# Kernel tuning notes

Measured on AMD Instinct MI355X. Metric: run time of the kernel, lower is better.

Reference implementation:

```python
import jax, jax.numpy as jnp
import numpy as np
import math

B, N, C = 8, 2048, 512

def setup_inputs() -> dict:
    key = jax.random.key(0)
    ks = jax.random.split(key, 7)
    s = 1.0 / math.sqrt(C)
    return {
        "feature": jax.random.normal(ks[0], (B, N, C), dtype=jnp.float32),
        "wq": jax.random.uniform(ks[1], (C, C), jnp.float32, -s, s),
        "bq": jax.random.uniform(ks[2], (C,), jnp.float32, -s, s),
        "wk": jax.random.uniform(ks[3], (C, C), jnp.float32, -s, s),
        "bk": jax.random.uniform(ks[4], (C,), jnp.float32, -s, s),
        "wv": jax.random.uniform(ks[5], (C, C), jnp.float32, -s, s),
        "bv": jax.random.uniform(ks[6], (C,), jnp.float32, -s, s),
    }

def reference(feature, wq, bq, wk, bk, wv, bv):
    # torch nn.Linear: x @ W.T + b
    q = jnp.einsum('bnc,dc->bnd', feature, wq) + bq
    k = jnp.einsum('bnc,dc->bnd', feature, wk) + bk
    v = jnp.einsum('bnc,dc->bnd', feature, wv) + bv
    scores = jnp.einsum('bnd,bmd->bnm', q, k)          # [B, N, N]
    attn = jax.nn.softmax(scores, axis=2) / math.sqrt(C)  # post-softmax scale (as in source)
    v_star = jnp.einsum('bnm,bmd->bnd', attn, v)
    return feature + v_star
```

## Files before the change

kernel.cpp:

```cpp
#include <hip/hip_runtime.h>
#include <cstdint>
#include <cstddef>


typedef __bf16 bf16x8 __attribute__((ext_vector_type(8)));
typedef float f32x4 __attribute__((ext_vector_type(4)));
typedef short short4v __attribute__((ext_vector_type(4)));
typedef short short8v __attribute__((ext_vector_type(8)));

__device__ __forceinline__ float b2f(short s) {
  union { float f; unsigned u; } u; u.u = ((unsigned)(unsigned short)s) << 16; return u.f;
}
__device__ __forceinline__ short f2b(float f) {
  union { float f; unsigned u; } u; u.f = f;
  unsigned r = (u.u + 0x7fffu + ((u.u >> 16) & 1u)) >> 16;
  return (short)r;
}

#define GLDS(gptr, lptr) \
  __builtin_amdgcn_global_load_lds( \
      (const __attribute__((address_space(1))) unsigned int*)(const void*)(gptr), \
      (__attribute__((address_space(3))) unsigned int*)(void*)(lptr), 16, 0, 0)

__global__ __launch_bounds__(256) void cvt_f32_bf16(const float* __restrict__ src,
                                                    short* __restrict__ dst, int n4) {
  int i = blockIdx.x * 256 + threadIdx.x;
  if (i >= n4) return;
  float4 f = ((const float4*)src)[i];
  short4v o = { f2b(f.x), f2b(f.y), f2b(f.z), f2b(f.w) };
  *(short4v*)(dst + (size_t)i * 4) = o;
}

__global__ __launch_bounds__(256) void cvt_w3(const float* __restrict__ w0,
                                              const float* __restrict__ w1,
                                              const float* __restrict__ w2,
                                              short* __restrict__ dst) {
  int i = blockIdx.x * 256 + threadIdx.x;
  const float* src = (i < 65536) ? w0 : (i < 131072) ? w1 : w2;
  int loc = i & 65535;
  float4 f = ((const float4*)src)[loc];
  short4v o = { f2b(f.x), f2b(f.y), f2b(f.z), f2b(f.w) };
  *(short4v*)(dst + (size_t)i * 4) = o;
}

__global__ __launch_bounds__(256) void pack_bias(const float* __restrict__ b0,
                                                 const float* __restrict__ b1,
                                                 const float* __restrict__ b2,
                                                 float* __restrict__ dst) {
  int t = blockIdx.x * 256 + threadIdx.x;
  if (t >= 1536) return;
  const float* s = (t < 512) ? b0 : (t < 1024) ? b1 : b2;
  dst[t] = s[t & 511];
}

__global__ __launch_bounds__(256) void gemm_qkv(const short* __restrict__ A,
                                                const short* __restrict__ Wb,
                                                const float* __restrict__ biasP,
                                                short* __restrict__ Out) {
  __shared__ __align__(16) short As[128 * 32];
  __shared__ __align__(16) short Bs[128 * 32];
  const int z = blockIdx.z;
  const short* Bm = Wb + (size_t)z * 262144;
  const int m0 = blockIdx.y * 128, n0 = blockIdx.x * 128;
  const int t = threadIdx.x;
  const int lane = t & 63, w = t >> 6;
  const int wm = (w & 1) * 64, wn = (w >> 1) * 64;
  const int fr = lane & 15, fk = (lane >> 4) * 8;

  f32x4 acc[4][4] = {};
  const int c0 = t, c1 = t + 256;
  const int r0 = c0 >> 2, k80 = (c0 & 3) * 8;
  const int r1 = c1 >> 2, k81 = (c1 & 3) * 8;

  for (int k0 = 0; k0 < 512; k0 += 32) {
    __syncthreads();
    GLDS(A + (size_t)(m0 + r0) * 512 + k0 + k80, As + c0 * 8);
    GLDS(A + (size_t)(m0 + r1) * 512 + k0 + k81, As + c1 * 8);
    GLDS(Bm + (size_t)(n0 + r0) * 512 + k0 + k80, Bs + c0 * 8);
    GLDS(Bm + (size_t)(n0 + r1) * 512 + k0 + k81, Bs + c1 * 8);
    __syncthreads();
    bf16x8 a[4], b[4];
#pragma unroll
    for (int i = 0; i < 4; ++i) a[i] = *(const bf16x8*)(As + (wm + i * 16 + fr) * 32 + fk);
#pragma unroll
    for (int j = 0; j < 4; ++j) b[j] = *(const bf16x8*)(Bs + (wn + j * 16 + fr) * 32 + fk);
#pragma unroll
    for (int i = 0; i < 4; ++i)
#pragma unroll
      for (int j = 0; j < 4; ++j)
        acc[i][j] = __builtin_amdgcn_mfma_f32_16x16x32_bf16(a[i], b[j], acc[i][j], 0, 0, 0);
  }

  const int rq = (lane >> 4) * 4;
#pragma unroll
  for (int i = 0; i < 4; ++i)
#pragma unroll
    for (int j = 0; j < 4; ++j)
#pragma unroll
      for (int r = 0; r < 4; ++r) {
        int row = m0 + wm + i * 16 + rq + r;
        int col = n0 + wn + j * 16 + fr;
        Out[(size_t)z * 8388608 + (size_t)row * 512 + col] =
            f2b(acc[i][j][r] + biasP[z * 512 + col]);
      }
}

__global__ __launch_bounds__(256) void gemm_qk(const short* __restrict__ Q,
                                               const short* __restrict__ K,
                                               short* __restrict__ P,
                                               float* __restrict__ l) {
  __shared__ __align__(16) short As[128 * 32];
  __shared__ __align__(16) short Bs[128 * 32];
  const int z = blockIdx.z;
  const short* A = Q + (size_t)z * 2048 * 512;
  const short* Bm = K + (size_t)z * 2048 * 512;
  const int m0 = blockIdx.y * 128, n0 = blockIdx.x * 128;
  const int t = threadIdx.x;
  const int lane = t & 63, w = t >> 6;
  const int wm = (w & 1) * 64, wn = (w >> 1) * 64;
  const int fr = lane & 15, fk = (lane >> 4) * 8;

  f32x4 acc[4][4] = {};
  const int c0 = t, c1 = t + 256;
  const int r0 = c0 >> 2, k80 = (c0 & 3) * 8;
  const int r1 = c1 >> 2, k81 = (c1 & 3) * 8;

  for (int k0 = 0; k0 < 512; k0 += 32) {
    __syncthreads();
    GLDS(A + (size_t)(m0 + r0) * 512 + k0 + k80, As + c0 * 8);
    GLDS(A + (size_t)(m0 + r1) * 512 + k0 + k81, As + c1 * 8);
    GLDS(Bm + (size_t)(n0 + r0) * 512 + k0 + k80, Bs + c0 * 8);
    GLDS(Bm + (size_t)(n0 + r1) * 512 + k0 + k81, Bs + c1 * 8);
    __syncthreads();
    bf16x8 a[4], b[4];
#pragma unroll
    for (int i = 0; i < 4; ++i) a[i] = *(const bf16x8*)(As + (wm + i * 16 + fr) * 32 + fk);
#pragma unroll
    for (int j = 0; j < 4; ++j) b[j] = *(const bf16x8*)(Bs + (wn + j * 16 + fr) * 32 + fk);
#pragma unroll
    for (int i = 0; i < 4; ++i)
#pragma unroll
      for (int j = 0; j < 4; ++j)
        acc[i][j] = __builtin_amdgcn_mfma_f32_16x16x32_bf16(a[i], b[j], acc[i][j], 0, 0, 0);
  }

  const int rq = (lane >> 4) * 4;
  float rs[4][4];
#pragma unroll
  for (int i = 0; i < 4; ++i)
#pragma unroll
    for (int r = 0; r < 4; ++r) rs[i][r] = 0.f;

#pragma unroll
  for (int i = 0; i < 4; ++i)
#pragma unroll
    for (int j = 0; j < 4; ++j)
#pragma unroll
      for (int r = 0; r < 4; ++r) {
        int row = m0 + wm + i * 16 + rq + r;
        int col = n0 + wn + j * 16 + fr;
        float e = exp2f(acc[i][j][r] * 1.4426950408889634f);
        short eb = f2b(e);
        P[(size_t)z * 4194304 + (size_t)row * 2048 + col] = eb;
        rs[i][r] += b2f(eb);
      }
#pragma unroll
  for (int i = 0; i < 4; ++i)
#pragma unroll
    for (int r = 0; r < 4; ++r) {
#pragma unroll
      for (int m = 1; m < 16; m <<= 1) rs[i][r] += __shfl_xor(rs[i][r], m);
    }
  if (fr == 0) {
#pragma unroll
    for (int i = 0; i < 4; ++i)
#pragma unroll
      for (int r = 0; r < 4; ++r)
        atomicAdd(&l[z * 2048 + m0 + wm + i * 16 + rq + r], rs[i][r]);
  }
}

__global__ __launch_bounds__(256) void gemm_pv(const short* __restrict__ Pm,
                                               const short* __restrict__ Vt,
                                               const float* __restrict__ l,
                                               const float* __restrict__ resid,
                                               float* __restrict__ out, float scale) {
  __shared__ __align__(16) short As[64 * 32];
  __shared__ __align__(16) short Bs[128 * 32];
  const int z = blockIdx.z;
  const short* A = Pm + (size_t)z * 4194304;
  const short* Bm = Vt + (size_t)z * 1048576;
  const int m0 = blockIdx.y * 64, n0 = blockIdx.x * 128;
  const int t = threadIdx.x;
  const int lane = t & 63, w = t >> 6;
  const int wm = (w & 1) * 32, wn = (w >> 1) * 64;
  const int fr = lane & 15, fk = (lane >> 4) * 8;

  f32x4 acc[2][4] = {};
  const int ra = t >> 2, k8a = (t & 3) * 8;
  const int c0 = t, c1 = t + 256;
  const int r0 = c0 >> 2, k80 = (c0 & 3) * 8;
  const int r1 = c1 >> 2, k81 = (c1 & 3) * 8;

  for (int k0 = 0; k0 < 2048; k0 += 32) {
    __syncthreads();
    GLDS(A + (size_t)(m0 + ra) * 2048 + k0 + k8a, As + t * 8);
    GLDS(Bm + (size_t)(n0 + r0) * 2048 + k0 + k80, Bs + c0 * 8);
    GLDS(Bm + (size_t)(n0 + r1) * 2048 + k0 + k81, Bs + c1 * 8);
    __syncthreads();
    bf16x8 a[2], b[4];
#pragma unroll
    for (int i = 0; i < 2; ++i) a[i] = *(const bf16x8*)(As + (wm + i * 16 + fr) * 32 + fk);
#pragma unroll
    for (int j = 0; j < 4; ++j) b[j] = *(const bf16x8*)(Bs + (wn + j * 16 + fr) * 32 + fk);
#pragma unroll
    for (int i = 0; i < 2; ++i)
#pragma unroll
      for (int j = 0; j < 4; ++j)
        acc[i][j] = __builtin_amdgcn_mfma_f32_16x16x32_bf16(a[i], b[j], acc[i][j], 0, 0, 0);
  }

  const int rq = (lane >> 4) * 4;
#pragma unroll
  for (int i = 0; i < 2; ++i)
#pragma unroll
    for (int r = 0; r < 4; ++r) {
      int row = m0 + wm + i * 16 + rq + r;
      float linv = scale / l[z * 2048 + row];
#pragma unroll
      for (int j = 0; j < 4; ++j) {
        int col = n0 + wn + j * 16 + fr;
        size_t idx = (size_t)z * 1048576 + (size_t)row * 512 + col;
        out[idx] = resid[idx] + acc[i][j][r] * linv;
      }
    }
}

__global__ __launch_bounds__(256) void transpose64(const short* __restrict__ V,
                                                   short* __restrict__ Vt) {
  __shared__ short tile[64][72];
  const int b = blockIdx.z;
  const int d0 = blockIdx.x * 64, n0 = blockIdx.y * 64;
  const int t = threadIdx.x;
#pragma unroll
  for (int h = 0; h < 2; ++h) {
    int c = t + h * 256;
    int r = c >> 3, cj = (c & 7) * 8;
    short8v val = *(const short8v*)(V + ((size_t)(b * 2048 + n0 + r)) * 512 + d0 + cj);
#pragma unroll
    for (int j = 0; j < 8; ++j) tile[r][cj + j] = val[j];
  }
  __syncthreads();
#pragma unroll
  for (int h = 0; h < 2; ++h) {
    int c = t + h * 256;
    int dr = c >> 3, nj = (c & 7) * 8;
    short8v o;
#pragma unroll
    for (int j = 0; j < 8; ++j) o[j] = tile[nj + j][dr];
    *(short8v*)(Vt + ((size_t)b * 512 + d0 + dr) * 2048 + n0 + nj) = o;
  }
}

extern "C" void kernel_launch(void* const* d_in, const int* in_sizes, int n_in,
                              void* d_out, int out_size, void* d_ws, size_t ws_size,
                              hipStream_t stream) {
  const float* feature = (const float*)d_in[0];
  const float* wq = (const float*)d_in[1];
  const float* bq = (const float*)d_in[2];
  const float* wk = (const float*)d_in[3];
  const float* bk = (const float*)d_in[4];
  const float* wv = (const float*)d_in[5];
  const float* bv = (const float*)d_in[6];
  float* out = (float*)d_out;

  const size_t MN = (size_t)16384 * 512;
  short* Xb = (short*)d_ws;
  short* Wb = Xb + MN;
  short* Q = Wb + 786432;
  short* K = Q + MN;
  short* V = K + MN;
  short* Vt = V + MN;
  short* P = Vt + MN;
  float* biasP = (float*)(P + (size_t)8 * 2048 * 2048);
  float* l = biasP + 1536;

  cvt_f32_bf16<<<8192, 256, 0, stream>>>(feature, Xb, 2097152);
  cvt_w3<<<768, 256, 0, stream>>>(wq, wk, wv, Wb);
  pack_bias<<<6, 256, 0, stream>>>(bq, bk, bv, biasP);
  hipMemsetAsync(l, 0, 16384 * sizeof(float), stream);

  gemm_qkv<<<dim3(4, 128, 3), 256, 0, stream>>>(Xb, Wb, biasP, Q);
  transpose64<<<dim3(8, 32, 8), 256, 0, stream>>>(V, Vt);
  gemm_qk<<<dim3(16, 16, 8), 256, 0, stream>>>(Q, K, P, l);

  const float iscl = 0.044194173824159216f;
  gemm_pv<<<dim3(4, 32, 8), 256, 0, stream>>>(P, Vt, l, feature, out, iscl);
}
```

Before: 277.3 us.

## Swap MFMA operands for vectorized row-contiguous epilogue stores and fuse prep kernels

Merges the three conversion/bias kernels and the memset into one prep launch, removing several launches. In the three GEMMs it swaps the MFMA A/B operands so each lane's four accumulator values lie along contiguous output columns. This allows 8-byte bf16 and 16-byte float4 epilogue stores and loads instead of scalar strided ones. The row-sum reduction in gemm_qk now needs only two shuffles plus atomics from 16 lanes.

```diff
diff --git a/kernel.cpp b/kernel.cpp
--- a/kernel.cpp
+++ b/kernel.cpp
@@ -22,49 +22,52 @@
       (const __attribute__((address_space(1))) unsigned int*)(const void*)(gptr), \
       (__attribute__((address_space(3))) unsigned int*)(void*)(lptr), 16, 0, 0)
 
-__global__ __launch_bounds__(256) void cvt_f32_bf16(const float* __restrict__ src,
-                                                    short* __restrict__ dst, int n4) {
-  int i = blockIdx.x * 256 + threadIdx.x;
-  if (i >= n4) return;
-  float4 f = ((const float4*)src)[i];
-  short4v o = { f2b(f.x), f2b(f.y), f2b(f.z), f2b(f.w) };
-  *(short4v*)(dst + (size_t)i * 4) = o;
-}
-
-__global__ __launch_bounds__(256) void cvt_w3(const float* __restrict__ w0,
-                                              const float* __restrict__ w1,
-                                              const float* __restrict__ w2,
-                                              short* __restrict__ dst) {
-  int i = blockIdx.x * 256 + threadIdx.x;
-  const float* src = (i < 65536) ? w0 : (i < 131072) ? w1 : w2;
-  int loc = i & 65535;
-  float4 f = ((const float4*)src)[loc];
-  short4v o = { f2b(f.x), f2b(f.y), f2b(f.z), f2b(f.w) };
-  *(short4v*)(dst + (size_t)i * 4) = o;
-}
-
-__global__ __launch_bounds__(256) void pack_bias(const float* __restrict__ b0,
-                                                 const float* __restrict__ b1,
-                                                 const float* __restrict__ b2,
-                                                 float* __restrict__ dst) {
-  int t = blockIdx.x * 256 + threadIdx.x;
-  if (t >= 1536) return;
-  const float* s = (t < 512) ? b0 : (t < 1024) ? b1 : b2;
-  dst[t] = s[t & 511];
-}
-
-__global__ __launch_bounds__(256) void gemm_qkv(const short* __restrict__ A,
-                                                const short* __restrict__ Wb,
+__global__ __launch_bounds__(256) void prep(const float* __restrict__ f,
+                                            const float* __restrict__ w0,
+                                            const float* __restrict__ w1,
+                                            const float* __restrict__ w2,
+                                            const float* __restrict__ b0,
+                                            const float* __restrict__ b1,
+                                            const float* __restrict__ b2,
+                                            short* __restrict__ Xb, short* __restrict__ Wb,
+                                            float* __restrict__ biasP, float* __restrict__ l) {
+  const int bid = blockIdx.x;
+  const int t = threadIdx.x;
+  if (bid < 8192) {
+    int i = bid * 256 + t;
+    float4 v = ((const float4*)f)[i];
+    short4v o = { f2b(v.x), f2b(v.y), f2b(v.z), f2b(v.w) };
+    *(short4v*)(Xb + (size_t)i * 4) = o;
+  } else if (bid < 8960) {
+    int i = (bid - 8192) * 256 + t;
+    const float* src = (i < 65536) ? w0 : (i < 131072) ? w1 : w2;
+    float4 v = ((const float4*)src)[i & 65535];
+    short4v o = { f2b(v.x), f2b(v.y), f2b(v.z), f2b(v.w) };
+    *(short4v*)(Wb + (size_t)i * 4) = o;
+  } else {
+    int i = (bid - 8960) * 256 + t;
+    float4 z = { 0.f, 0.f, 0.f, 0.f };
+    ((float4*)l)[i * 2] = z;
+    ((float4*)l)[i * 2 + 1] = z;
+    if (i < 1536) {
+      const float* s = (i < 512) ? b0 : (i < 1024) ? b1 : b2;
+      biasP[i] = s[i & 511];
+    }
+  }
+}
+
+__global__ __launch_bounds__(256) void gemm_qkv(const short* __restrict__ X,
+                                                const short* __restrict__ Wall,
                                                 const float* __restrict__ biasP,
                                                 short* __restrict__ Out) {
-  __shared__ __align__(16) short As[128 * 32];
-  __shared__ __align__(16) short Bs[128 * 32];
+  __shared__ __align__(16) short Xs[128 * 32];
+  __shared__ __align__(16) short Ws[128 * 32];
   const int z = blockIdx.z;
-  const short* Bm = Wb + (size_t)z * 262144;
+  const short* Wm = Wall + (size_t)z * 262144;
   const int m0 = blockIdx.y * 128, n0 = blockIdx.x * 128;
   const int t = threadIdx.x;
   const int lane = t & 63, w = t >> 6;
-  const int wm = (w & 1) * 64, wn = (w >> 1) * 64;
+  const int wn = (w & 1) * 64, wm = (w >> 1) * 64;
   const int fr = lane & 15, fk = (lane >> 4) * 8;
 
   f32x4 acc[4][4] = {};
@@ -74,50 +77,51 @@
 
   for (int k0 = 0; k0 < 512; k0 += 32) {
     __syncthreads();
-    GLDS(A + (size_t)(m0 + r0) * 512 + k0 + k80, As + c0 * 8);
-    GLDS(A + (size_t)(m0 + r1) * 512 + k0 + k81, As + c1 * 8);
-    GLDS(Bm + (size_t)(n0 + r0) * 512 + k0 + k80, Bs + c0 * 8);
-    GLDS(Bm + (size_t)(n0 + r1) * 512 + k0 + k81, Bs + c1 * 8);
-    __syncthreads();
-    bf16x8 a[4], b[4];
-#pragma unroll
-    for (int i = 0; i < 4; ++i) a[i] = *(const bf16x8*)(As + (wm + i * 16 + fr) * 32 + fk);
-#pragma unroll
-    for (int j = 0; j < 4; ++j) b[j] = *(const bf16x8*)(Bs + (wn + j * 16 + fr) * 32 + fk);
+    GLDS(X + (size_t)(m0 + r0) * 512 + k0 + k80, Xs + c0 * 8);
+    GLDS(X + (size_t)(m0 + r1) * 512 + k0 + k81, Xs + c1 * 8);
+    GLDS(Wm + (size_t)(n0 + r0) * 512 + k0 + k80, Ws + c0 * 8);
+    GLDS(Wm + (size_t)(n0 + r1) * 512 + k0 + k81, Ws + c1 * 8);
+    __syncthreads();
+    bf16x8 wf[4], xf[4];
+#pragma unroll
+    for (int i = 0; i < 4; ++i) wf[i] = *(const bf16x8*)(Ws + (wn + i * 16 + fr) * 32 + fk);
+#pragma unroll
+    for (int j = 0; j < 4; ++j) xf[j] = *(const bf16x8*)(Xs + (wm + j * 16 + fr) * 32 + fk);
 #pragma unroll
     for (int i = 0; i < 4; ++i)
 #pragma unroll
       for (int j = 0; j < 4; ++j)
-        acc[i][j] = __builtin_amdgcn_mfma_f32_16x16x32_bf16(a[i], b[j], acc[i][j], 0, 0, 0);
+        acc[i][j] = __builtin_amdgcn_mfma_f32_16x16x32_bf16(wf[i], xf[j], acc[i][j], 0, 0, 0);
   }
 
   const int rq = (lane >> 4) * 4;
 #pragma unroll
-  for (int i = 0; i < 4; ++i)
-#pragma unroll
-    for (int j = 0; j < 4; ++j)
-#pragma unroll
-      for (int r = 0; r < 4; ++r) {
-        int row = m0 + wm + i * 16 + rq + r;
-        int col = n0 + wn + j * 16 + fr;
-        Out[(size_t)z * 8388608 + (size_t)row * 512 + col] =
-            f2b(acc[i][j][r] + biasP[z * 512 + col]);
-      }
+  for (int i = 0; i < 4; ++i) {
+    int nb = n0 + wn + i * 16 + rq;
+    float4 bs = *(const float4*)(biasP + z * 512 + nb);
+#pragma unroll
+    for (int j = 0; j < 4; ++j) {
+      int m = m0 + wm + j * 16 + fr;
+      short4v o = { f2b(acc[i][j][0] + bs.x), f2b(acc[i][j][1] + bs.y),
+                    f2b(acc[i][j][2] + bs.z), f2b(acc[i][j][3] + bs.w) };
+      *(short4v*)(Out + (size_t)z * 8388608 + (size_t)m * 512 + nb) = o;
+    }
+  }
 }
 
 __global__ __launch_bounds__(256) void gemm_qk(const short* __restrict__ Q,
-                                               const short* __restrict__ K,
+                                               const short* __restrict__ Kb,
                                                short* __restrict__ P,
                                                float* __restrict__ l) {
-  __shared__ __align__(16) short As[128 * 32];
-  __shared__ __align__(16) short Bs[128 * 32];
+  __shared__ __align__(16) short Qs[128 * 32];
+  __shared__ __align__(16) short Ks[128 * 32];
   const int z = blockIdx.z;
   const short* A = Q + (size_t)z * 2048 * 512;
-  const short* Bm = K + (size_t)z * 2048 * 512;
+  const short* Bm = Kb + (size_t)z * 2048 * 512;
   const int m0 = blockIdx.y * 128, n0 = blockIdx.x * 128;
   const int t = threadIdx.x;
   const int lane = t & 63, w = t >> 6;
-  const int wm = (w & 1) * 64, wn = (w >> 1) * 64;
+  const int wn = (w & 1) * 64, wm = (w >> 1) * 64;
   const int fr = lane & 15, fk = (lane >> 4) * 8;
 
   f32x4 acc[4][4] = {};
@@ -127,56 +131,53 @@
 
   for (int k0 = 0; k0 < 512; k0 += 32) {
     __syncthreads();
-    GLDS(A + (size_t)(m0 + r0) * 512 + k0 + k80, As + c0 * 8);
-    GLDS(A + (size_t)(m0 + r1) * 512 + k0 + k81, As + c1 * 8);
-    GLDS(Bm + (size_t)(n0 + r0) * 512 + k0 + k80, Bs + c0 * 8);
-    GLDS(Bm + (size_t)(n0 + r1) * 512 + k0 + k81, Bs + c1 * 8);
-    __syncthreads();
-    bf16x8 a[4], b[4];
-#pragma unroll
-    for (int i = 0; i < 4; ++i) a[i] = *(const bf16x8*)(As + (wm + i * 16 + fr) * 32 + fk);
-#pragma unroll
-    for (int j = 0; j < 4; ++j) b[j] = *(const bf16x8*)(Bs + (wn + j * 16 + fr) * 32 + fk);
+    GLDS(A + (size_t)(m0 + r0) * 512 + k0 + k80, Qs + c0 * 8);
+    GLDS(A + (size_t)(m0 + r1) * 512 + k0 + k81, Qs + c1 * 8);
+    GLDS(Bm + (size_t)(n0 + r0) * 512 + k0 + k80, Ks + c0 * 8);
+    GLDS(Bm + (size_t)(n0 + r1) * 512 + k0 + k81, Ks + c1 * 8);
+    __syncthreads();
+    bf16x8 kf[4], qf[4];
+#pragma unroll
+    for (int i = 0; i < 4; ++i) kf[i] = *(const bf16x8*)(Ks + (wn + i * 16 + fr) * 32 + fk);
+#pragma unroll
+    for (int j = 0; j < 4; ++j) qf[j] = *(const bf16x8*)(Qs + (wm + j * 16 + fr) * 32 + fk);
 #pragma unroll
     for (int i = 0; i < 4; ++i)
 #pragma unroll
       for (int j = 0; j < 4; ++j)
-        acc[i][j] = __builtin_amdgcn_mfma_f32_16x16x32_bf16(a[i], b[j], acc[i][j], 0, 0, 0);
+        acc[i][j] = __builtin_amdgcn_mfma_f32_16x16x32_bf16(kf[i], qf[j], acc[i][j], 0, 0, 0);
   }
 
   const int rq = (lane >> 4) * 4;
-  float rs[4][4];
-#pragma unroll
-  for (int i = 0; i < 4; ++i)
-#pragma unroll
-    for (int r = 0; r < 4; ++r) rs[i][r] = 0.f;
-
-#pragma unroll
-  for (int i = 0; i < 4; ++i)
-#pragma unroll
-    for (int j = 0; j < 4; ++j)
+  float rs[4] = { 0.f, 0.f, 0.f, 0.f };
+#pragma unroll
+  for (int i = 0; i < 4; ++i) {
+    int nb = n0 + wn + i * 16 + rq;
+#pragma unroll
+    for (int j = 0; j < 4; ++j) {
+      int m = m0 + wm + j * 16 + fr;
+      short4v o;
+      float part = 0.f;
 #pragma unroll
       for (int r = 0; r < 4; ++r) {
-        int row = m0 + wm + i * 16 + rq + r;
-        int col = n0 + wn + j * 16 + fr;
         float e = exp2f(acc[i][j][r] * 1.4426950408889634f);
         short eb = f2b(e);
-        P[(size_t)z * 4194304 + (size_t)row * 2048 + col] = eb;
-        rs[i][r] += b2f(eb);
+        o[r] = eb;
+        part += b2f(eb);
       }
-#pragma unroll
-  for (int i = 0; i < 4; ++i)
-#pragma unroll
-    for (int r = 0; r < 4; ++r) {
-#pragma unroll
-      for (int m = 1; m < 16; m <<= 1) rs[i][r] += __shfl_xor(rs[i][r], m);
-    }
-  if (fr == 0) {
-#pragma unroll
-    for (int i = 0; i < 4; ++i)
-#pragma unroll
-      for (int r = 0; r < 4; ++r)
-        atomicAdd(&l[z * 2048 + m0 + wm + i * 16 + rq + r], rs[i][r]);
+      *(short4v*)(P + (size_t)z * 4194304 + (size_t)m * 2048 + nb) = o;
+      rs[j] += part;
+    }
+  }
+#pragma unroll
+  for (int j = 0; j < 4; ++j) {
+    rs[j] += __shfl_xor(rs[j], 16);
+    rs[j] += __shfl_xor(rs[j], 32);
+  }
+  if (lane < 16) {
+#pragma unroll
+    for (int j = 0; j < 4; ++j)
+      atomicAdd(&l[z * 2048 + m0 + wm + j * 16 + fr], rs[j]);
   }
 }
 
@@ -185,18 +186,18 @@
                                                const float* __restrict__ l,
                                                const float* __restrict__ resid,
                                                float* __restrict__ out, float scale) {
-  __shared__ __align__(16) short As[64 * 32];
-  __shared__ __align__(16) short Bs[128 * 32];
+  __shared__ __align__(16) short Ps[64 * 32];
+  __shared__ __align__(16) short Vs[128 * 32];
   const int z = blockIdx.z;
   const short* A = Pm + (size_t)z * 4194304;
   const short* Bm = Vt + (size_t)z * 1048576;
   const int m0 = blockIdx.y * 64, n0 = blockIdx.x * 128;
   const int t = threadIdx.x;
   const int lane = t & 63, w = t >> 6;
-  const int wm = (w & 1) * 32, wn = (w >> 1) * 64;
+  const int wn = (w & 1) * 64, wm = (w >> 1) * 32;
   const int fr = lane & 15, fk = (lane >> 4) * 8;
 
-  f32x4 acc[2][4] = {};
+  f32x4 acc[4][2] = {};
   const int ra = t >> 2, k8a = (t & 3) * 8;
   const int c0 = t, c1 = t + 256;
   const int r0 = c0 >> 2, k80 = (c0 & 3) * 8;
@@ -204,36 +205,37 @@
 
   for (int k0 = 0; k0 < 2048; k0 += 32) {
     __syncthreads();
-    GLDS(A + (size_t)(m0 + ra) * 2048 + k0 + k8a, As + t * 8);
-    GLDS(Bm + (size_t)(n0 + r0) * 2048 + k0 + k80, Bs + c0 * 8);
-    GLDS(Bm + (size_t)(n0 + r1) * 2048 + k0 + k81, Bs + c1 * 8);
-    __syncthreads();
-    bf16x8 a[2], b[4];
-#pragma unroll
-    for (int i = 0; i < 2; ++i) a[i] = *(const bf16x8*)(As + (wm + i * 16 + fr) * 32 + fk);
-#pragma unroll
-    for (int j = 0; j < 4; ++j) b[j] = *(const bf16x8*)(Bs + (wn + j * 16 + fr) * 32 + fk);
-#pragma unroll
-    for (int i = 0; i < 2; ++i)
-#pragma unroll
-      for (int j = 0; j < 4; ++j)
-        acc[i][j] = __builtin_amdgcn_mfma_f32_16x16x32_bf16(a[i], b[j], acc[i][j], 0, 0, 0);
+    GLDS(A + (size_t)(m0 + ra) * 2048 + k0 + k8a, Ps + t * 8);
+    GLDS(Bm + (size_t)(n0 + r0) * 2048 + k0 + k80, Vs + c0 * 8);
+    GLDS(Bm + (size_t)(n0 + r1) * 2048 + k0 + k81, Vs + c1 * 8);
+    __syncthreads();
+    bf16x8 vf[4], pf[2];
+#pragma unroll
+    for (int i = 0; i < 4; ++i) vf[i] = *(const bf16x8*)(Vs + (wn + i * 16 + fr) * 32 + fk);
+#pragma unroll
+    for (int j = 0; j < 2; ++j) pf[j] = *(const bf16x8*)(Ps + (wm + j * 16 + fr) * 32 + fk);
+#pragma unroll
+    for (int i = 0; i < 4; ++i)
+#pragma unroll
+      for (int j = 0; j < 2; ++j)
+        acc[i][j] = __builtin_amdgcn_mfma_f32_16x16x32_bf16(vf[i], pf[j], acc[i][j], 0, 0, 0);
   }
 
   const int rq = (lane >> 4) * 4;
 #pragma unroll
-  for (int i = 0; i < 2; ++i)
-#pragma unroll
-    for (int r = 0; r < 4; ++r) {
-      int row = m0 + wm + i * 16 + rq + r;
-      float linv = scale / l[z * 2048 + row];
-#pragma unroll
-      for (int j = 0; j < 4; ++j) {
-        int col = n0 + wn + j * 16 + fr;
-        size_t idx = (size_t)z * 1048576 + (size_t)row * 512 + col;
-        out[idx] = resid[idx] + acc[i][j][r] * linv;
-      }
-    }
+  for (int j = 0; j < 2; ++j) {
+    int m = m0 + wm + j * 16 + fr;
+    float linv = scale / l[z * 2048 + m];
+#pragma unroll
+    for (int i = 0; i < 4; ++i) {
+      int nb = n0 + wn + i * 16 + rq;
+      size_t idx = (size_t)z * 1048576 + (size_t)m * 512 + nb;
+      float4 rv = *(const float4*)(resid + idx);
+      float4 o = { rv.x + acc[i][j][0] * linv, rv.y + acc[i][j][1] * linv,
+                   rv.z + acc[i][j][2] * linv, rv.w + acc[i][j][3] * linv };
+      *(float4*)(out + idx) = o;
+    }
+  }
 }
 
 __global__ __launch_bounds__(256) void transpose64(const short* __restrict__ V,
@@ -285,10 +287,7 @@
   float* biasP = (float*)(P + (size_t)8 * 2048 * 2048);
   float* l = biasP + 1536;
 
-  cvt_f32_bf16<<<8192, 256, 0, stream>>>(feature, Xb, 2097152);
-  cvt_w3<<<768, 256, 0, stream>>>(wq, wk, wv, Wb);
-  pack_bias<<<6, 256, 0, stream>>>(bq, bk, bv, biasP);
-  hipMemsetAsync(l, 0, 16384 * sizeof(float), stream);
+  prep<<<8968, 256, 0, stream>>>(feature, wq, wk, wv, bq, bk, bv, Xb, Wb, biasP, l);
 
   gemm_qkv<<<dim3(4, 128, 3), 256, 0, stream>>>(Xb, Wb, biasP, Q);
   transpose64<<<dim3(8, 32, 8), 256, 0, stream>>>(V, Vt);
```

Measured after the change: 270.6 us. 2.4% less time.
